# Kernel optimization log

Measured on AMD Instinct MI355X. Metric: run time of the kernel, lower is better.

## Reference

```python
import jax, jax.numpy as jnp
import numpy as np
from jax import lax

EXPANDED_BASE_DIM = 256
VISUAL_FEATURE_DIM = 768
HIDDEN_DIM = 1024
INPUT_DIM = EXPANDED_BASE_DIM + VISUAL_FEATURE_DIM
B, K = 256, 128


def setup_inputs() -> dict:
    key = jax.random.key(0)
    k1, k2, k3, k4, k5, k6 = jax.random.split(key, 6)
    s = 1.0 / np.sqrt(HIDDEN_DIM)  # PyTorch GRU init scale
    return {
        "base_expanded_seq": jax.random.normal(k1, (B, K, EXPANDED_BASE_DIM), jnp.float32),
        "visual_seq": jax.random.normal(k2, (B, K, VISUAL_FEATURE_DIM), jnp.float32),
        # PyTorch layout: gates stacked as [r, z, n] along first axis (3H)
        "W_ih": jax.random.uniform(k3, (3 * HIDDEN_DIM, INPUT_DIM), jnp.float32, -s, s),
        "W_hh": jax.random.uniform(k4, (3 * HIDDEN_DIM, HIDDEN_DIM), jnp.float32, -s, s),
        "b_ih": jax.random.uniform(k5, (3 * HIDDEN_DIM,), jnp.float32, -s, s),
        "b_hh": jax.random.uniform(k6, (3 * HIDDEN_DIM,), jnp.float32, -s, s),
    }


def reference(base_expanded_seq, visual_seq, W_ih, W_hh, b_ih, b_hh):
    # Faithful to GRUEncoder.forward: per-step concat -> GRU cell, return final h.
    x_seq = jnp.concatenate([base_expanded_seq, visual_seq], axis=-1)  # (B,K,I)
    Bb, Kk, _ = x_seq.shape
    H = W_hh.shape[1]
    # Precompute input projections for all steps (same math, batched GEMM)
    x_proj = jnp.einsum('bki,gi->bkg', x_seq, W_ih) + b_ih  # (B,K,3H)
    x_proj_t = jnp.swapaxes(x_proj, 0, 1)  # (K,B,3H)

    def step(h, xp):
        hp = h @ W_hh.T + b_hh  # (B,3H)
        xr, xz, xn = jnp.split(xp, 3, axis=-1)
        hr, hz, hn = jnp.split(hp, 3, axis=-1)
        r = jax.nn.sigmoid(xr + hr)
        z = jax.nn.sigmoid(xz + hz)
        n = jnp.tanh(xn + r * hn)
        h_new = (1.0 - z) * n + z * h
        return h_new, None

    h0 = jnp.zeros((Bb, H), x_seq.dtype)
    h_final, _ = lax.scan(step, h0, x_proj_t)
    return h_final  # (B, H) == h[-1] for num_layers=1
```

## Files before the change

### kernel.cpp

```cpp
#include <hip/hip_runtime.h>

#define BATCH 256
#define SEQ   128
#define IDIM  1024
#define HDIM  1024
#define G3    3072

typedef __attribute__((ext_vector_type(8))) short bf16x8;
typedef __attribute__((ext_vector_type(4))) short s16x4;
typedef __attribute__((ext_vector_type(4))) float f32x4;

__device__ __forceinline__ short f2bf(float f) {
    union { float f; unsigned u; } x; x.f = f;
    unsigned r = x.u + 0x7fffu + ((x.u >> 16) & 1u);
    return (short)(r >> 16);
}
__device__ __forceinline__ float bf2f(unsigned short u) {
    union { unsigned u; float f; } x; x.u = ((unsigned)u) << 16;
    return x.f;
}

__device__ __forceinline__ void st_llc_b64(short* p, s16x4 v) {
    asm volatile("global_store_dwordx2 %0, %1, off sc0 sc1" :: "v"(p), "v"(v) : "memory");
}
#define LDH(dst, p, OFF) \
    asm volatile("global_load_dwordx4 %0, %1, off offset:" OFF " sc0 sc1" \
                 : "=v"(dst) : "v"(p))

__global__ void cvt_w(const float* __restrict__ wih, const float* __restrict__ whh,
                      short* __restrict__ wihb, short* __restrict__ whhb) {
    int i = blockIdx.x * 256 + threadIdx.x;
    const float* s; short* d; int j;
    if (i < 786432) { s = wih; d = wihb; j = i; }
    else            { s = whh; d = whhb; j = i - 786432; }
    const float4 v = *((const float4*)s + j);
    s16x4 o;
    o[0] = f2bf(v.x); o[1] = f2bf(v.y); o[2] = f2bf(v.z); o[3] = f2bf(v.w);
    *(s16x4*)(d + (size_t)j * 4) = o;
}

__global__ __launch_bounds__(256, 2) void gemm_xproj(
    const float* __restrict__ base, const float* __restrict__ vis,
    const short* __restrict__ wihb, const float* __restrict__ bih,
    short* __restrict__ xp)
{
    __shared__ short As[128 * 64];
    __shared__ short Bs[128 * 64];
    const int tid = threadIdx.x;
    const int bid = blockIdx.x;
    const int nt = bid % 24, mt = bid / 24;
    const int m0 = mt * 128, n0 = nt * 128;
    const int lane = tid & 63, w = tid >> 6;
    const int wm = w >> 1, wn = w & 1;
    const int l15 = lane & 15, quad = lane >> 4;

    f32x4 acc[4][4];
#pragma unroll
    for (int i = 0; i < 4; ++i)
#pragma unroll
        for (int j = 0; j < 4; ++j) acc[i][j] = (f32x4){0.f, 0.f, 0.f, 0.f};

    const int arow = tid >> 3;
    const int acol8 = (tid & 7) * 8;

    for (int kt = 0; kt < 16; ++kt) {
        const int k0 = kt * 64;
        __syncthreads();
#pragma unroll
        for (int is = 0; is < 4; ++is) {
            const int row = is * 32 + arow;
            const int col = k0 + acol8;
            const float* s = (col < 256)
                ? (base + (size_t)(m0 + row) * 256 + col)
                : (vis  + (size_t)(m0 + row) * 768 + (col - 256));
            const float4 v0 = *(const float4*)s;
            const float4 v1 = *(const float4*)(s + 4);
            bf16x8 pk;
            pk[0] = f2bf(v0.x); pk[1] = f2bf(v0.y); pk[2] = f2bf(v0.z); pk[3] = f2bf(v0.w);
            pk[4] = f2bf(v1.x); pk[5] = f2bf(v1.y); pk[6] = f2bf(v1.z); pk[7] = f2bf(v1.w);
            *(bf16x8*)&As[is * 2048 + tid * 8] = pk;
            __builtin_amdgcn_global_load_lds(
                (const __attribute__((address_space(1))) void*)(wihb + (size_t)(n0 + is * 32 + (tid >> 3)) * 1024 + k0 + (tid & 7) * 8),
                (__attribute__((address_space(3))) void*)&Bs[is * 2048 + tid * 8],
                16, 0, 0);
        }
        __syncthreads();
#pragma unroll
        for (int s2 = 0; s2 < 2; ++s2) {
            bf16x8 af[4], bf[4];
#pragma unroll
            for (int i = 0; i < 4; ++i)
                af[i] = *(const bf16x8*)&As[(wm * 64 + i * 16 + l15) * 64 + s2 * 32 + quad * 8];
#pragma unroll
            for (int j = 0; j < 4; ++j)
                bf[j] = *(const bf16x8*)&Bs[(wn * 64 + j * 16 + l15) * 64 + s2 * 32 + quad * 8];
#pragma unroll
            for (int i = 0; i < 4; ++i)
#pragma unroll
                for (int j = 0; j < 4; ++j)
                    acc[i][j] = __builtin_amdgcn_mfma_f32_16x16x32_bf16(af[i], bf[j], acc[i][j], 0, 0, 0);
        }
    }
#pragma unroll
    for (int j = 0; j < 4; ++j) {
        const int gn = n0 + wn * 64 + j * 16 + l15;
        const float bv = bih[gn];
#pragma unroll
        for (int i = 0; i < 4; ++i) {
            const int gmb = m0 + wm * 64 + i * 16 + quad * 4;
#pragma unroll
            for (int r = 0; r < 4; ++r) {
                const int gm = gmb + r;
                const size_t off = ((size_t)(gm & 127) * 256 + (size_t)(gm >> 7)) * 3072 + gn;
                xp[off] = f2bf(acc[i][j][r] + bv);
            }
        }
    }
}

__global__ __launch_bounds__(256, 1) void gru_rec(
    const short* __restrict__ xp, const short* __restrict__ whhb,
    const float* __restrict__ bhh, short* __restrict__ hbuf,
    float* __restrict__ out, unsigned* __restrict__ ctr)
{
    __shared__ float red[4 * 32 * 96];
    const int tid = threadIdx.x;
    const int bid = blockIdx.x;
    const int bt = bid >> 5;
    const int ct = bid & 31;
    const int lane = tid & 63, w = tid >> 6;
    const int l15 = lane & 15, quad = lane >> 4;
    const int bm0 = bt * 32;
    const int kbase = w * 256 + quad * 8;

    bf16x8 Bf[6][8];
#pragma unroll
    for (int g = 0; g < 6; ++g) {
        const size_t col = (size_t)((g >> 1) * 1024 + ct * 32 + (g & 1) * 16 + l15);
#pragma unroll
        for (int kk = 0; kk < 8; ++kk)
            Bf[g][kk] = *(const bf16x8*)(whhb + col * 1024 + kbase + kk * 32);
    }

    const int er = tid >> 3;
    const int ec0 = (tid & 7) * 4;
    const f32x4 bhr = *(const f32x4*)(bhh + ct * 32 + ec0);
    const f32x4 bhz = *(const f32x4*)(bhh + 1024 + ct * 32 + ec0);
    const f32x4 bhn = *(const f32x4*)(bhh + 2048 + ct * 32 + ec0);

    float hold[4] = {0.f, 0.f, 0.f, 0.f};
    s16x4 xc[3], xn_[3];
    {
        const size_t rb = (size_t)(bm0 + er) * 3072 + ct * 32 + ec0;
#pragma unroll
        for (int g = 0; g < 3; ++g) xc[g] = *(const s16x4*)(xp + rb + g * 1024);
    }

    for (int step = 0; step < 128; ++step) {
        const short* hr_ = hbuf + (size_t)(step & 1) * (256 * 1024);
        short* hw_ = hbuf + (size_t)((step + 1) & 1) * (256 * 1024);

        bf16x8 A0[8], A1[8];
        const short* p0 = hr_ + (size_t)(bm0 + l15) * 1024 + kbase;
        const short* p1 = p0 + 16 * 1024;
        LDH(A0[0], p0, "0");   LDH(A0[1], p0, "64");  LDH(A0[2], p0, "128"); LDH(A0[3], p0, "192");
        LDH(A0[4], p0, "256"); LDH(A0[5], p0, "320"); LDH(A0[6], p0, "384"); LDH(A0[7], p0, "448");
        LDH(A1[0], p1, "0");   LDH(A1[1], p1, "64");  LDH(A1[2], p1, "128"); LDH(A1[3], p1, "192");
        LDH(A1[4], p1, "256"); LDH(A1[5], p1, "320"); LDH(A1[6], p1, "384"); LDH(A1[7], p1, "448");
        asm volatile("s_waitcnt vmcnt(0)"
            : "+v"(A0[0]), "+v"(A0[1]), "+v"(A0[2]), "+v"(A0[3]),
              "+v"(A0[4]), "+v"(A0[5]), "+v"(A0[6]), "+v"(A0[7]),
              "+v"(A1[0]), "+v"(A1[1]), "+v"(A1[2]), "+v"(A1[3]),
              "+v"(A1[4]), "+v"(A1[5]), "+v"(A1[6]), "+v"(A1[7])
            :: "memory");

        f32x4 acc[2][6];
#pragma unroll
        for (int i = 0; i < 2; ++i)
#pragma unroll
            for (int g = 0; g < 6; ++g) acc[i][g] = (f32x4){0.f, 0.f, 0.f, 0.f};

#pragma unroll
        for (int kk = 0; kk < 8; ++kk) {
#pragma unroll
            for (int g = 0; g < 6; ++g) {
                acc[0][g] = __builtin_amdgcn_mfma_f32_16x16x32_bf16(A0[kk], Bf[g][kk], acc[0][g], 0, 0, 0);
                acc[1][g] = __builtin_amdgcn_mfma_f32_16x16x32_bf16(A1[kk], Bf[g][kk], acc[1][g], 0, 0, 0);
            }
        }
#pragma unroll
        for (int i = 0; i < 2; ++i)
#pragma unroll
            for (int g = 0; g < 6; ++g) {
                const int c96 = (g >> 1) * 32 + (g & 1) * 16 + l15;
                const int rb = w * 32 + i * 16 + quad * 4;
#pragma unroll
                for (int r = 0; r < 4; ++r)
                    red[(rb + r) * 96 + c96] = acc[i][g][r];
            }
        if (step < 127) {
            const size_t rb = ((size_t)(step + 1) * 256 + bm0 + er) * 3072 + ct * 32 + ec0;
#pragma unroll
            for (int g = 0; g < 3; ++g) xn_[g] = *(const s16x4*)(xp + rb + g * 1024);
        }
        __syncthreads();
        f32x4 sr = bhr, sz = bhz, sn = bhn;
#pragma unroll
        for (int ww = 0; ww < 4; ++ww) {
            const float* rbp = &red[(ww * 32 + er) * 96];
            sr += *(const f32x4*)(rbp + ec0);
            sz += *(const f32x4*)(rbp + 32 + ec0);
            sn += *(const f32x4*)(rbp + 64 + ec0);
        }
        s16x4 hpk;
        float ov[4];
#pragma unroll
        for (int i = 0; i < 4; ++i) {
            const float xr = bf2f((unsigned short)xc[0][i]);
            const float xz = bf2f((unsigned short)xc[1][i]);
            const float xnv = bf2f((unsigned short)xc[2][i]);
            const float rg = 1.f / (1.f + __expf(-(xr + sr[i])));
            const float zg = 1.f / (1.f + __expf(-(xz + sz[i])));
            const float e2 = __expf(2.f * (xnv + rg * sn[i]));
            const float ng = 1.f - 2.f / (e2 + 1.f);
            const float hv = (1.f - zg) * ng + zg * hold[i];
            hold[i] = hv; ov[i] = hv;
            hpk[i] = f2bf(hv);
        }
        st_llc_b64(&hw_[(size_t)(bm0 + er) * 1024 + ct * 32 + ec0], hpk);
        (void)ov;
        if (step < 127) {
            asm volatile("s_waitcnt vmcnt(0)" ::: "memory");
            __syncthreads();
            if (tid == 0) {
                const int ci = bt * 128 + step;
                __hip_atomic_fetch_add(&ctr[ci], 1u, __ATOMIC_RELAXED, __HIP_MEMORY_SCOPE_AGENT);
                while (__hip_atomic_load(&ctr[ci], __ATOMIC_RELAXED, __HIP_MEMORY_SCOPE_AGENT) < 32u)
                    __builtin_amdgcn_s_sleep(1);
            }
            __syncthreads();
#pragma unroll
            for (int g = 0; g < 3; ++g) xc[g] = xn_[g];
        }
    }
    float4 o4; o4.x = hold[0]; o4.y = hold[1]; o4.z = hold[2]; o4.w = hold[3];
    *(float4*)(out + (size_t)(bm0 + er) * 1024 + ct * 32 + ec0) = o4;
}

extern "C" void kernel_launch(void* const* d_in, const int* in_sizes, int n_in,
                              void* d_out, int out_size, void* d_ws, size_t ws_size,
                              hipStream_t stream) {
    (void)in_sizes; (void)n_in; (void)out_size; (void)ws_size;
    const float* base = (const float*)d_in[0];
    const float* vis  = (const float*)d_in[1];
    const float* wih  = (const float*)d_in[2];
    const float* whh  = (const float*)d_in[3];
    const float* bih  = (const float*)d_in[4];
    const float* bhh  = (const float*)d_in[5];

    char* ws = (char*)d_ws;
    short*    xp   = (short*)(ws + 0);
    short*    wihb = (short*)(ws + 201326592);
    short*    whhb = (short*)(ws + 207618048);
    short*    hbuf = (short*)(ws + 213909504);
    unsigned* ctr  = (unsigned*)(ws + 214958080);

    hipMemsetAsync(hbuf, 0, 1048576, stream);
    hipMemsetAsync(ctr, 0, 4096, stream);

    cvt_w<<<dim3(6144), dim3(256), 0, stream>>>(wih, whh, wihb, whhb);
    gemm_xproj<<<dim3(6144), dim3(256), 0, stream>>>(base, vis, wihb, bih, xp);
    gru_rec<<<dim3(256), dim3(256), 0, stream>>>(xp, whhb, bhh, hbuf, (float*)d_out, ctr);
}
```

Before: 1.287 ms.

## Replace atomic counter barrier with per-block flags and stage GEMM output via LDS

```diff
diff --git a/kernel.cpp b/kernel.cpp
--- a/kernel.cpp
+++ b/kernel.cpp
@@ -5,6 +5,7 @@
 #define IDIM  1024
 #define HDIM  1024
 #define G3    3072
+#define RS    100
 
 typedef __attribute__((ext_vector_type(8))) short bf16x8;
 typedef __attribute__((ext_vector_type(4))) short s16x4;
@@ -23,9 +24,14 @@
 __device__ __forceinline__ void st_llc_b64(short* p, s16x4 v) {
     asm volatile("global_store_dwordx2 %0, %1, off sc0 sc1" :: "v"(p), "v"(v) : "memory");
 }
+__device__ __forceinline__ void st_llc_b32(unsigned* p, unsigned v) {
+    asm volatile("global_store_dword %0, %1, off sc0 sc1" :: "v"(p), "v"(v) : "memory");
+}
 #define LDH(dst, p, OFF) \
     asm volatile("global_load_dwordx4 %0, %1, off offset:" OFF " sc0 sc1" \
                  : "=v"(dst) : "v"(p))
+#define LDX(dst, p) \
+    asm volatile("global_load_dwordx2 %0, %1, off" : "=v"(dst) : "v"(p))
 
 __global__ void cvt_w(const float* __restrict__ wih, const float* __restrict__ whh,
                       short* __restrict__ wihb, short* __restrict__ whhb) {
@@ -44,8 +50,10 @@
     const short* __restrict__ wihb, const float* __restrict__ bih,
     short* __restrict__ xp)
 {
-    __shared__ short As[128 * 64];
-    __shared__ short Bs[128 * 64];
+    __shared__ union {
+        struct { short A[128 * 64]; short B[128 * 64]; } ab;
+        short C[128 * 136];
+    } sm;
     const int tid = threadIdx.x;
     const int bid = blockIdx.x;
     const int nt = bid % 24, mt = bid / 24;
@@ -78,10 +86,10 @@
             bf16x8 pk;
             pk[0] = f2bf(v0.x); pk[1] = f2bf(v0.y); pk[2] = f2bf(v0.z); pk[3] = f2bf(v0.w);
             pk[4] = f2bf(v1.x); pk[5] = f2bf(v1.y); pk[6] = f2bf(v1.z); pk[7] = f2bf(v1.w);
-            *(bf16x8*)&As[is * 2048 + tid * 8] = pk;
+            *(bf16x8*)&sm.ab.A[is * 2048 + tid * 8] = pk;
             __builtin_amdgcn_global_load_lds(
                 (const __attribute__((address_space(1))) void*)(wihb + (size_t)(n0 + is * 32 + (tid >> 3)) * 1024 + k0 + (tid & 7) * 8),
-                (__attribute__((address_space(3))) void*)&Bs[is * 2048 + tid * 8],
+                (__attribute__((address_space(3))) void*)&sm.ab.B[is * 2048 + tid * 8],
                 16, 0, 0);
         }
         __syncthreads();
@@ -90,10 +98,10 @@
             bf16x8 af[4], bf[4];
 #pragma unroll
             for (int i = 0; i < 4; ++i)
-                af[i] = *(const bf16x8*)&As[(wm * 64 + i * 16 + l15) * 64 + s2 * 32 + quad * 8];
+                af[i] = *(const bf16x8*)&sm.ab.A[(wm * 64 + i * 16 + l15) * 64 + s2 * 32 + quad * 8];
 #pragma unroll
             for (int j = 0; j < 4; ++j)
-                bf[j] = *(const bf16x8*)&Bs[(wn * 64 + j * 16 + l15) * 64 + s2 * 32 + quad * 8];
+                bf[j] = *(const bf16x8*)&sm.ab.B[(wn * 64 + j * 16 + l15) * 64 + s2 * 32 + quad * 8];
 #pragma unroll
             for (int i = 0; i < 4; ++i)
 #pragma unroll
@@ -101,29 +109,37 @@
                     acc[i][j] = __builtin_amdgcn_mfma_f32_16x16x32_bf16(af[i], bf[j], acc[i][j], 0, 0, 0);
         }
     }
+    __syncthreads();
 #pragma unroll
     for (int j = 0; j < 4; ++j) {
-        const int gn = n0 + wn * 64 + j * 16 + l15;
-        const float bv = bih[gn];
+        const int cn = wn * 64 + j * 16 + l15;
+        const float bv = bih[n0 + cn];
 #pragma unroll
         for (int i = 0; i < 4; ++i) {
-            const int gmb = m0 + wm * 64 + i * 16 + quad * 4;
-#pragma unroll
-            for (int r = 0; r < 4; ++r) {
-                const int gm = gmb + r;
-                const size_t off = ((size_t)(gm & 127) * 256 + (size_t)(gm >> 7)) * 3072 + gn;
-                xp[off] = f2bf(acc[i][j][r] + bv);
-            }
-        }
+            const int rb = wm * 64 + i * 16 + quad * 4;
+#pragma unroll
+            for (int r = 0; r < 4; ++r)
+                sm.C[(rb + r) * 136 + cn] = f2bf(acc[i][j][r] + bv);
+        }
+    }
+    __syncthreads();
+    {
+        const int row = tid >> 1, c0 = (tid & 1) * 64;
+        const int gm = m0 + row;
+        short* dst = xp + ((size_t)(gm & 127) * 256 + (size_t)(gm >> 7)) * 3072 + n0 + c0;
+        const short* src = &sm.C[row * 136 + c0];
+#pragma unroll
+        for (int c = 0; c < 64; c += 8)
+            *(bf16x8*)(dst + c) = *(const bf16x8*)(src + c);
     }
 }
 
 __global__ __launch_bounds__(256, 1) void gru_rec(
     const short* __restrict__ xp, const short* __restrict__ whhb,
     const float* __restrict__ bhh, short* __restrict__ hbuf,
-    float* __restrict__ out, unsigned* __restrict__ ctr)
+    float* __restrict__ out, unsigned* __restrict__ flags)
 {
-    __shared__ float red[4 * 32 * 96];
+    __shared__ float red[128 * RS];
     const int tid = threadIdx.x;
     const int bid = blockIdx.x;
     const int bt = bid >> 5;
@@ -148,6 +164,9 @@
     const f32x4 bhz = *(const f32x4*)(bhh + 1024 + ct * 32 + ec0);
     const f32x4 bhn = *(const f32x4*)(bhh + 2048 + ct * 32 + ec0);
 
+    unsigned* const myflag = flags + bt * 32 + ct;
+    const unsigned* const pollp = flags + bt * 32 + (lane & 31);
+
     float hold[4] = {0.f, 0.f, 0.f, 0.f};
     s16x4 xc[3], xn_[3];
     {
@@ -157,6 +176,14 @@
     }
 
     for (int step = 0; step < 128; ++step) {
+        if (step > 0) {
+            const unsigned tgt = (unsigned)step;
+            unsigned fv;
+            do {
+                asm volatile("global_load_dword %0, %1, off sc0 sc1" : "=v"(fv) : "v"(pollp));
+                asm volatile("s_waitcnt vmcnt(0)" : "+v"(fv) :: "memory");
+            } while (__ballot(fv < tgt));
+        }
         const short* hr_ = hbuf + (size_t)(step & 1) * (256 * 1024);
         short* hw_ = hbuf + (size_t)((step + 1) & 1) * (256 * 1024);
 
@@ -173,13 +200,16 @@
               "+v"(A1[0]), "+v"(A1[1]), "+v"(A1[2]), "+v"(A1[3]),
               "+v"(A1[4]), "+v"(A1[5]), "+v"(A1[6]), "+v"(A1[7])
             :: "memory");
+        if (step < 127) {
+            const short* rb = xp + ((size_t)(step + 1) * 256 + bm0 + er) * 3072 + ct * 32 + ec0;
+            LDX(xn_[0], rb); LDX(xn_[1], rb + 1024); LDX(xn_[2], rb + 2048);
+        }
 
         f32x4 acc[2][6];
 #pragma unroll
         for (int i = 0; i < 2; ++i)
 #pragma unroll
             for (int g = 0; g < 6; ++g) acc[i][g] = (f32x4){0.f, 0.f, 0.f, 0.f};
-
 #pragma unroll
         for (int kk = 0; kk < 8; ++kk) {
 #pragma unroll
@@ -196,24 +226,18 @@
                 const int rb = w * 32 + i * 16 + quad * 4;
 #pragma unroll
                 for (int r = 0; r < 4; ++r)
-                    red[(rb + r) * 96 + c96] = acc[i][g][r];
+                    red[(rb + r) * RS + c96] = acc[i][g][r];
             }
-        if (step < 127) {
-            const size_t rb = ((size_t)(step + 1) * 256 + bm0 + er) * 3072 + ct * 32 + ec0;
-#pragma unroll
-            for (int g = 0; g < 3; ++g) xn_[g] = *(const s16x4*)(xp + rb + g * 1024);
-        }
         __syncthreads();
         f32x4 sr = bhr, sz = bhz, sn = bhn;
 #pragma unroll
         for (int ww = 0; ww < 4; ++ww) {
-            const float* rbp = &red[(ww * 32 + er) * 96];
+            const float* rbp = &red[(ww * 32 + er) * RS];
             sr += *(const f32x4*)(rbp + ec0);
             sz += *(const f32x4*)(rbp + 32 + ec0);
             sn += *(const f32x4*)(rbp + 64 + ec0);
         }
         s16x4 hpk;
-        float ov[4];
 #pragma unroll
         for (int i = 0; i < 4; ++i) {
             const float xr = bf2f((unsigned short)xc[0][i]);
@@ -224,23 +248,18 @@
             const float e2 = __expf(2.f * (xnv + rg * sn[i]));
             const float ng = 1.f - 2.f / (e2 + 1.f);
             const float hv = (1.f - zg) * ng + zg * hold[i];
-            hold[i] = hv; ov[i] = hv;
+            hold[i] = hv;
             hpk[i] = f2bf(hv);
         }
-        st_llc_b64(&hw_[(size_t)(bm0 + er) * 1024 + ct * 32 + ec0], hpk);
-        (void)ov;
         if (step < 127) {
-            asm volatile("s_waitcnt vmcnt(0)" ::: "memory");
+            st_llc_b64(&hw_[(size_t)(bm0 + er) * 1024 + ct * 32 + ec0], hpk);
+            asm volatile("s_waitcnt vmcnt(0)"
+                : "+v"(xn_[0]), "+v"(xn_[1]), "+v"(xn_[2]) :: "memory");
             __syncthreads();
-            if (tid == 0) {
-                const int ci = bt * 128 + step;
-                __hip_atomic_fetch_add(&ctr[ci], 1u, __ATOMIC_RELAXED, __HIP_MEMORY_SCOPE_AGENT);
-                while (__hip_atomic_load(&ctr[ci], __ATOMIC_RELAXED, __HIP_MEMORY_SCOPE_AGENT) < 32u)
-                    __builtin_amdgcn_s_sleep(1);
-            }
+            if (tid == 0) st_llc_b32(myflag, (unsigned)(step + 1));
+            xc[0] = xn_[0]; xc[1] = xn_[1]; xc[2] = xn_[2];
+        } else {
             __syncthreads();
-#pragma unroll
-            for (int g = 0; g < 3; ++g) xc[g] = xn_[g];
         }
     }
     float4 o4; o4.x = hold[0]; o4.y = hold[1]; o4.z = hold[2]; o4.w = hold[3];
@@ -263,12 +282,12 @@
     short*    wihb = (short*)(ws + 201326592);
     short*    whhb = (short*)(ws + 207618048);
     short*    hbuf = (short*)(ws + 213909504);
-    unsigned* ctr  = (unsigned*)(ws + 214958080);
+    unsigned* flg  = (unsigned*)(ws + 214958080);
 
     hipMemsetAsync(hbuf, 0, 1048576, stream);
-    hipMemsetAsync(ctr, 0, 4096, stream);
+    hipMemsetAsync(flg, 0, 4096, stream);
 
     cvt_w<<<dim3(6144), dim3(256), 0, stream>>>(wih, whh, wihb, whhb);
     gemm_xproj<<<dim3(6144), dim3(256), 0, stream>>>(base, vis, wihb, bih, xp);
-    gru_rec<<<dim3(256), dim3(256), 0, stream>>>(xp, whhb, bhh, hbuf, (float*)d_out, ctr);
-}
+    gru_rec<<<dim3(256), dim3(256), 0, stream>>>(xp, whhb, bhh, hbuf, (float*)d_out, flg);
+}
```

Result: faster. 1.195 ms (-7.2%).
